# Optimization experiments

Hardware: AMD Instinct MI355X
Metric: run time of the kernel (lower is better)

The kernel has to match this reference:

```python
import jax, jax.numpy as jnp
import numpy as np

B, S, D, H = 2, 2048, 2048, 16
DH = D // H  # 128 head dim
ROPE_THETA = 10000.0
LN_EPS = 1e-5


def setup_inputs() -> dict:
    key = jax.random.key(0)
    k1, k2, k3 = jax.random.split(key, 3)
    positions = jnp.broadcast_to(jnp.arange(S, dtype=jnp.int64), (B, S))
    hidden_states = jax.random.normal(k1, (B, S, D), dtype=jnp.float32)
    w_qkv = jax.random.normal(k2, (D, 3 * D), dtype=jnp.float32) * 0.02
    w_out = jax.random.normal(k3, (D, D), dtype=jnp.float32) * 0.02
    return {"positions": positions, "hidden_states": hidden_states,
            "w_qkv": w_qkv, "w_out": w_out}


def _rope(x, positions):
    # NeoX-style rotary (vLLM get_rope default): rotate split halves.
    # x: [B, S, H, DH], positions: [B, S]
    half = DH // 2
    inv_freq = 1.0 / (ROPE_THETA ** (jnp.arange(0, half, dtype=jnp.float32) / half))
    ang = positions.astype(jnp.float32)[..., None] * inv_freq  # [B, S, half]
    cos = jnp.cos(ang)[:, :, None, :]  # [B, S, 1, half]
    sin = jnp.sin(ang)[:, :, None, :]
    x1, x2 = x[..., :half], x[..., half:]
    return jnp.concatenate([x1 * cos - x2 * sin, x2 * cos + x1 * sin], axis=-1)


def reference(positions, hidden_states, w_qkv, w_out):
    # LayerNorm with no affine params (elementwise_affine=False)
    mu = jnp.mean(hidden_states, axis=-1, keepdims=True)
    var = jnp.mean(jnp.square(hidden_states - mu), axis=-1, keepdims=True)
    x = (hidden_states - mu) * jax.lax.rsqrt(var + LN_EPS)

    qkv = jnp.einsum('bsd,de->bse', x, w_qkv)  # [B, S, 3D]
    q, k, v = jnp.split(qkv, 3, axis=-1)
    q = q.reshape(B, S, H, DH)
    k = k.reshape(B, S, H, DH)
    v = v.reshape(B, S, H, DH)

    q = _rope(q, positions)
    k = _rope(k, positions)

    scale = DH ** -0.5
    scores = jnp.einsum('bqhd,bkhd->bhqk', q, k) * scale  # [B, H, S, S]
    causal = jnp.tril(jnp.ones((S, S), dtype=bool))
    scores = jnp.where(causal, scores, jnp.finfo(scores.dtype).min)
    probs = jax.nn.softmax(scores, axis=-1)
    attn = jnp.einsum('bhqk,bkhd->bqhd', probs, v).reshape(B, S, D)

    return jnp.einsum('bsd,de->bse', attn, w_out)
```

## Files before the change

kernel.cpp:

```cpp
#include <hip/hip_runtime.h>


typedef __bf16 bf16x8 __attribute__((ext_vector_type(8)));
typedef float f32x4 __attribute__((ext_vector_type(4)));

__device__ __forceinline__ unsigned short f2bf(float f) {
  unsigned u = __builtin_bit_cast(unsigned, f);
  u = u + 0x7fffu + ((u >> 16) & 1u);
  return (unsigned short)(u >> 16);
}
__device__ __forceinline__ float bf2f(unsigned short h) {
  unsigned u = ((unsigned)h) << 16;
  return __builtin_bit_cast(float, u);
}

#define GLD_LDS16(gp, lp)                                                      \
  __builtin_amdgcn_global_load_lds((__attribute__((address_space(1))) void*)(gp), \
                                   (__attribute__((address_space(3))) void*)(lp), \
                                   16, 0, 0)

__global__ __launch_bounds__(256) void ln_kernel(const float* __restrict__ hs,
                                                 unsigned short* __restrict__ xb) {
  const int row = blockIdx.x;
  const int tid = threadIdx.x;
  const float* rp = hs + (size_t)row * 2048;
  const float4 v0 = ((const float4*)rp)[tid];
  const float4 v1 = ((const float4*)rp)[tid + 256];
  float s  = v0.x + v0.y + v0.z + v0.w + v1.x + v1.y + v1.z + v1.w;
  float ss = v0.x*v0.x + v0.y*v0.y + v0.z*v0.z + v0.w*v0.w
           + v1.x*v1.x + v1.y*v1.y + v1.z*v1.z + v1.w*v1.w;
#pragma unroll
  for (int m = 1; m < 64; m <<= 1) { s += __shfl_xor(s, m); ss += __shfl_xor(ss, m); }
  __shared__ float rs[4], rss[4];
  if ((tid & 63) == 0) { rs[tid >> 6] = s; rss[tid >> 6] = ss; }
  __syncthreads();
  s  = rs[0] + rs[1] + rs[2] + rs[3];
  ss = rss[0] + rss[1] + rss[2] + rss[3];
  const float mean = s * (1.0f / 2048.0f);
  const float var  = ss * (1.0f / 2048.0f) - mean * mean;
  const float inv  = rsqrtf(var + 1e-5f);
  ushort4 o0, o1;
  o0.x = f2bf((v0.x - mean) * inv); o0.y = f2bf((v0.y - mean) * inv);
  o0.z = f2bf((v0.z - mean) * inv); o0.w = f2bf((v0.w - mean) * inv);
  o1.x = f2bf((v1.x - mean) * inv); o1.y = f2bf((v1.y - mean) * inv);
  o1.z = f2bf((v1.z - mean) * inv); o1.w = f2bf((v1.w - mean) * inv);
  ushort4* op = (ushort4*)(xb + (size_t)row * 2048);
  op[tid] = o0; op[tid + 256] = o1;
}

__global__ __launch_bounds__(256) void cast_transpose(const float* __restrict__ in,
                                                      unsigned short* __restrict__ out,
                                                      int K, int N) {
  __shared__ float t[32][33];
  const int n0 = blockIdx.x * 32, k0 = blockIdx.y * 32;
  const int tx = threadIdx.x, ty = threadIdx.y;
#pragma unroll
  for (int i = 0; i < 4; i++)
    t[ty + i * 8][tx] = in[(size_t)(k0 + ty + i * 8) * N + n0 + tx];
  __syncthreads();
#pragma unroll
  for (int i = 0; i < 4; i++)
    out[(size_t)(n0 + ty + i * 8) * K + k0 + tx] = f2bf(t[tx][ty + i * 8]);
}

template <int OUT_BF16>
__global__ __launch_bounds__(256) void gemm_bt(const unsigned short* __restrict__ A,
                                               const unsigned short* __restrict__ Bt,
                                               void* __restrict__ Cv,
                                               int M, int N, int K) {
  __shared__ alignas(16) unsigned short sA[128 * 32];
  __shared__ alignas(16) unsigned short sB[128 * 32];
  const int tid = threadIdx.x;
  const int lane = tid & 63, wave = tid >> 6;
  const int wm = wave >> 1, wn = wave & 1;
  const int ln15 = lane & 15, quad = lane >> 4;
  const size_t m0 = (size_t)blockIdx.y * 128, n0 = (size_t)blockIdx.x * 128;
  const unsigned short* Ag = A + m0 * (size_t)K;
  const unsigned short* Bg = Bt + n0 * (size_t)K;
  const int c0 = wave * 2, c1 = wave * 2 + 1;
  const int lr = lane >> 2;
  const int scw = ((lane & 3) ^ ((lr >> 1) & 3)) * 8;
  const int rsw = (ln15 >> 1) & 3;

  f32x4 acc[4][4];
#pragma unroll
  for (int mi = 0; mi < 4; mi++)
#pragma unroll
    for (int ni = 0; ni < 4; ni++) acc[mi][ni] = (f32x4){0.f, 0.f, 0.f, 0.f};

  const int iters = K >> 5;
  for (int kt = 0; kt < iters; ++kt) {
    const int kb = kt * 32;
    __syncthreads();
    GLD_LDS16(Ag + (size_t)(c0 * 16 + lr) * K + kb + scw, &sA[c0 * 512]);
    GLD_LDS16(Ag + (size_t)(c1 * 16 + lr) * K + kb + scw, &sA[c1 * 512]);
    GLD_LDS16(Bg + (size_t)(c0 * 16 + lr) * K + kb + scw, &sB[c0 * 512]);
    GLD_LDS16(Bg + (size_t)(c1 * 16 + lr) * K + kb + scw, &sB[c1 * 512]);
    __syncthreads();
    bf16x8 af[4], bf[4];
#pragma unroll
    for (int mi = 0; mi < 4; mi++)
      af[mi] = *(const bf16x8*)&sA[(wm * 64 + mi * 16 + ln15) * 32 + (quad ^ rsw) * 8];
#pragma unroll
    for (int ni = 0; ni < 4; ni++)
      bf[ni] = *(const bf16x8*)&sB[(wn * 64 + ni * 16 + ln15) * 32 + (quad ^ rsw) * 8];
#pragma unroll
    for (int mi = 0; mi < 4; mi++)
#pragma unroll
      for (int ni = 0; ni < 4; ni++)
        acc[mi][ni] = __builtin_amdgcn_mfma_f32_16x16x32_bf16(af[mi], bf[ni], acc[mi][ni], 0, 0, 0);
  }
#pragma unroll
  for (int mi = 0; mi < 4; mi++)
#pragma unroll
    for (int ni = 0; ni < 4; ni++) {
      const size_t col = n0 + wn * 64 + ni * 16 + ln15;
#pragma unroll
      for (int r = 0; r < 4; r++) {
        const size_t row = m0 + wm * 64 + mi * 16 + quad * 4 + r;
        if (OUT_BF16)
          ((unsigned short*)Cv)[row * N + col] = f2bf(acc[mi][ni][r]);
        else
          ((float*)Cv)[row * N + col] = acc[mi][ni][r];
      }
    }
}

__global__ __launch_bounds__(256) void rope_kernel(const unsigned short* __restrict__ qkv,
                                                   unsigned short* __restrict__ Qo,
                                                   unsigned short* __restrict__ Ko) {
  const int t = blockIdx.x * 256 + threadIdx.x;
  const int i = t & 63;
  const int h = (t >> 6) & 15;
  const int row = t >> 10;
  const int s = row & 2047;
  const float freq = exp2f(-(float)i * (13.287712379549449f / 64.0f));
  const float ang = (float)s * freq;
  float rev = ang * 0.15915494309189535f;
  rev -= floorf(rev);
  const float ar = rev * 6.283185307179586f;
  const float sn = __sinf(ar), cs = __cosf(ar);
  const float qscale = 0.08838834764831845f;
  const size_t base = (size_t)row * 6144 + h * 128;
  const float q1 = bf2f(qkv[base + i]);
  const float q2 = bf2f(qkv[base + 64 + i]);
  const float k1 = bf2f(qkv[base + 2048 + i]);
  const float k2 = bf2f(qkv[base + 2048 + 64 + i]);
  const size_t ob = ((size_t)(((row >> 11) << 4) + h) * 2048 + s) * 128;
  Qo[ob + i]      = f2bf((q1 * cs - q2 * sn) * qscale);
  Qo[ob + 64 + i] = f2bf((q2 * cs + q1 * sn) * qscale);
  Ko[ob + i]      = f2bf(k1 * cs - k2 * sn);
  Ko[ob + 64 + i] = f2bf(k2 * cs + k1 * sn);
}

__global__ __launch_bounds__(256) void vtrans_kernel(const unsigned short* __restrict__ qkv,
                                                     unsigned short* __restrict__ VT) {
  __shared__ unsigned short t[32][34];
  const int s0 = blockIdx.x * 32, d0 = blockIdx.y * 32;
  const int bh = blockIdx.z, b = bh >> 4, h = bh & 15;
  const int tx = threadIdx.x, ty = threadIdx.y;
#pragma unroll
  for (int i = 0; i < 4; i++)
    t[ty + i * 8][tx] =
        qkv[(size_t)(b * 2048 + s0 + ty + i * 8) * 6144 + 4096 + h * 128 + d0 + tx];
  __syncthreads();
#pragma unroll
  for (int i = 0; i < 4; i++)
    VT[((size_t)bh * 128 + d0 + ty + i * 8) * 2048 + s0 + tx] = t[tx][ty + i * 8];
}

__global__ __launch_bounds__(256) void flash_kernel(const unsigned short* __restrict__ Q,
                                                    const unsigned short* __restrict__ Kbuf,
                                                    const unsigned short* __restrict__ VT,
                                                    unsigned short* __restrict__ attn) {
  __shared__ alignas(16) unsigned short sK[64 * 128];
  __shared__ alignas(16) unsigned short sVT[128 * 64];
  __shared__ alignas(16) unsigned short sP[64 * 72];

  const int bh = blockIdx.y;
  const int b = bh >> 4, h = bh & 15;
  const int tid = threadIdx.x;
  const int lane = tid & 63, w = tid >> 6;
  const int ln15 = lane & 15, quad = lane >> 4;

  const unsigned short* Qg = Q + (size_t)bh * 2048 * 128;
  const unsigned short* Kg = Kbuf + (size_t)bh * 2048 * 128;
  const unsigned short* Vg = VT + (size_t)bh * 128 * 2048;

  const float L2E = 1.44269504088896f;

#pragma unroll 1
  for (int t = 0; t < 2; t++) {
    const int qt = t ? (31 - (int)blockIdx.x) : (int)blockIdx.x;
    const int q0 = qt * 64;

    bf16x8 qf[4];
#pragma unroll
    for (int ks = 0; ks < 4; ks++)
      qf[ks] = *(const bf16x8*)&Qg[(size_t)(q0 + w * 16 + ln15) * 128 + ks * 32 + quad * 8];

    f32x4 o[8];
#pragma unroll
    for (int nd = 0; nd < 8; nd++) o[nd] = (f32x4){0.f, 0.f, 0.f, 0.f};
    float mrow[4], lrow[4];
#pragma unroll
    for (int r = 0; r < 4; r++) { mrow[r] = -1e30f; lrow[r] = 0.f; }

#pragma unroll 1
    for (int j = 0; j <= qt; j++) {
      const int k0 = j * 64;
      __syncthreads();
#pragma unroll
      for (int i = 0; i < 4; i++) {
        const int c = w * 4 + i;
        const int row = c * 4 + (lane >> 4);
        const int ch = (lane & 15) ^ (row & 15);
        GLD_LDS16(Kg + (size_t)(k0 + row) * 128 + ch * 8, &sK[c * 512]);
      }
#pragma unroll
      for (int i = 0; i < 4; i++) {
        const int c = w * 4 + i;
        const int row = c * 8 + (lane >> 3);
        const int ch = (lane & 7) ^ (row & 7);
        GLD_LDS16(Vg + (size_t)row * 2048 + k0 + ch * 8, &sVT[c * 512]);
      }
      __syncthreads();

      f32x4 sc[4];
#pragma unroll
      for (int ni = 0; ni < 4; ni++) sc[ni] = (f32x4){0.f, 0.f, 0.f, 0.f};
#pragma unroll
      for (int ks = 0; ks < 4; ks++) {
        bf16x8 bk[4];
#pragma unroll
        for (int ni = 0; ni < 4; ni++) {
          const int row = ni * 16 + ln15;
          const int ch = (ks * 4 + quad) ^ (row & 15);
          bk[ni] = *(const bf16x8*)&sK[row * 128 + ch * 8];
        }
#pragma unroll
        for (int ni = 0; ni < 4; ni++)
          sc[ni] = __builtin_amdgcn_mfma_f32_16x16x32_bf16(qf[ks], bk[ni], sc[ni], 0, 0, 0);
      }

      float mt[4] = {-1e30f, -1e30f, -1e30f, -1e30f};
      if (j == qt) {
#pragma unroll
        for (int ni = 0; ni < 4; ni++) {
          const int key = k0 + ni * 16 + ln15;
#pragma unroll
          for (int r = 0; r < 4; r++) {
            const int qrow = q0 + w * 16 + quad * 4 + r;
            float v = sc[ni][r];
            if (key > qrow) v = -1e30f;
            sc[ni][r] = v;
            mt[r] = fmaxf(mt[r], v);
          }
        }
      } else {
#pragma unroll
        for (int ni = 0; ni < 4; ni++)
#pragma unroll
          for (int r = 0; r < 4; r++) mt[r] = fmaxf(mt[r], sc[ni][r]);
      }
#pragma unroll
      for (int r = 0; r < 4; r++) {
        float m = mt[r];
        m = fmaxf(m, __shfl_xor(m, 1));
        m = fmaxf(m, __shfl_xor(m, 2));
        m = fmaxf(m, __shfl_xor(m, 4));
        m = fmaxf(m, __shfl_xor(m, 8));
        const float mnew = fmaxf(mrow[r], m);
        const float alpha = exp2f((mrow[r] - mnew) * L2E);
        mrow[r] = mnew;
        float rs = 0.f;
#pragma unroll
        for (int ni = 0; ni < 4; ni++) {
          const float p = exp2f((sc[ni][r] - mnew) * L2E);
          sc[ni][r] = p;
          rs += p;
        }
        rs += __shfl_xor(rs, 1);
        rs += __shfl_xor(rs, 2);
        rs += __shfl_xor(rs, 4);
        rs += __shfl_xor(rs, 8);
        lrow[r] = lrow[r] * alpha + rs;
#pragma unroll
        for (int nd = 0; nd < 8; nd++) o[nd][r] *= alpha;
      }
#pragma unroll
      for (int ni = 0; ni < 4; ni++)
#pragma unroll
        for (int r = 0; r < 4; r++)
          sP[(w * 16 + quad * 4 + r) * 72 + ni * 16 + ln15] = f2bf(sc[ni][r]);

      bf16x8 pf[2];
#pragma unroll
      for (int kk = 0; kk < 2; kk++)
        pf[kk] = *(const bf16x8*)&sP[(w * 16 + ln15) * 72 + kk * 32 + quad * 8];
#pragma unroll
      for (int kk = 0; kk < 2; kk++)
#pragma unroll
        for (int nd = 0; nd < 8; nd++) {
          const int row = nd * 16 + ln15;
          const int ch = (kk * 4 + quad) ^ (row & 7);
          const bf16x8 bv = *(const bf16x8*)&sVT[row * 64 + ch * 8];
          o[nd] = __builtin_amdgcn_mfma_f32_16x16x32_bf16(pf[kk], bv, o[nd], 0, 0, 0);
        }
    }

#pragma unroll
    for (int r = 0; r < 4; r++) {
      const float inv = 1.0f / lrow[r];
      const int qrow = q0 + w * 16 + quad * 4 + r;
#pragma unroll
      for (int nd = 0; nd < 8; nd++) {
        const int d = nd * 16 + ln15;
        attn[((size_t)(b * 2048 + qrow)) * 2048 + h * 128 + d] = f2bf(o[nd][r] * inv);
      }
    }
  }
}

extern "C" void kernel_launch(void* const* d_in, const int* in_sizes, int n_in,
                              void* d_out, int out_size, void* d_ws, size_t ws_size,
                              hipStream_t stream) {
  const float* hs   = (const float*)d_in[1];
  const float* wqkv = (const float*)d_in[2];
  const float* wout = (const float*)d_in[3];
  float* out = (float*)d_out;
  char* ws = (char*)d_ws;

  unsigned short* x_bf  = (unsigned short*)(ws);
  unsigned short* wqkvT = (unsigned short*)(ws + 16777216);
  unsigned short* woutT = (unsigned short*)(ws + 41943040);
  unsigned short* qkv   = (unsigned short*)(ws + 50331648);
  unsigned short* Qb    = (unsigned short*)(ws + 100663296);
  unsigned short* Kb    = (unsigned short*)(ws + 117440512);
  unsigned short* VT    = wqkvT;
  unsigned short* attn  = x_bf;

  ln_kernel<<<4096, 256, 0, stream>>>(hs, x_bf);
  cast_transpose<<<dim3(192, 64), dim3(32, 8), 0, stream>>>(wqkv, wqkvT, 2048, 6144);
  cast_transpose<<<dim3(64, 64), dim3(32, 8), 0, stream>>>(wout, woutT, 2048, 2048);
  gemm_bt<1><<<dim3(48, 32), 256, 0, stream>>>(x_bf, wqkvT, (void*)qkv, 4096, 6144, 2048);
  rope_kernel<<<16384, 256, 0, stream>>>(qkv, Qb, Kb);
  vtrans_kernel<<<dim3(64, 4, 32), dim3(32, 8), 0, stream>>>(qkv, VT);
  flash_kernel<<<dim3(16, 32), 256, 0, stream>>>(Qb, Kb, VT, attn);
  gemm_bt<0><<<dim3(16, 32), 256, 0, stream>>>(attn, woutT, (void*)out, 4096, 2048, 2048);
}
```

Before: 446.9 us.

## Widen GEMM K-tile, vectorize RoPE, merge weight casts, MFMA row-sum in flash

The GEMM K-tile grows from 32 to 64 with a new XOR swizzle, which halves the barriers and global-load rounds per K step. RoPE now has each thread handle 8 contiguous elements with 16-byte loads and stores, cutting the grid from 16384 to 2048 blocks. The two weight cast-transpose launches become one kernel. In flash attention, the softmax row sum now comes from an extra MFMA against a ones vector instead of shuffle reductions, so it uses bf16-rounded P for the denominator and doubles GEMM LDS use.

Result: faster. 424.7 us (-5.0%).

```diff
diff --git a/kernel.cpp b/kernel.cpp
--- a/kernel.cpp
+++ b/kernel.cpp
@@ -48,11 +48,18 @@
   op[tid] = o0; op[tid + 256] = o1;
 }
 
-__global__ __launch_bounds__(256) void cast_transpose(const float* __restrict__ in,
-                                                      unsigned short* __restrict__ out,
-                                                      int K, int N) {
+__global__ __launch_bounds__(256) void cast_transpose2(const float* __restrict__ wqkv,
+                                                       const float* __restrict__ wout,
+                                                       unsigned short* __restrict__ wqkvT,
+                                                       unsigned short* __restrict__ woutT) {
   __shared__ float t[32][33];
-  const int n0 = blockIdx.x * 32, k0 = blockIdx.y * 32;
+  const int bx = blockIdx.x;
+  const float* in;
+  unsigned short* out;
+  int N, n0;
+  if (bx < 192) { in = wqkv; out = wqkvT; N = 6144; n0 = bx * 32; }
+  else          { in = wout; out = woutT; N = 2048; n0 = (bx - 192) * 32; }
+  const int k0 = blockIdx.y * 32;
   const int tx = threadIdx.x, ty = threadIdx.y;
 #pragma unroll
   for (int i = 0; i < 4; i++)
@@ -60,7 +67,7 @@
   __syncthreads();
 #pragma unroll
   for (int i = 0; i < 4; i++)
-    out[(size_t)(n0 + ty + i * 8) * K + k0 + tx] = f2bf(t[tx][ty + i * 8]);
+    out[(size_t)(n0 + ty + i * 8) * 2048 + k0 + tx] = f2bf(t[tx][ty + i * 8]);
 }
 
 template <int OUT_BF16>
@@ -68,8 +75,8 @@
                                                const unsigned short* __restrict__ Bt,
                                                void* __restrict__ Cv,
                                                int M, int N, int K) {
-  __shared__ alignas(16) unsigned short sA[128 * 32];
-  __shared__ alignas(16) unsigned short sB[128 * 32];
+  __shared__ alignas(16) unsigned short sA[128 * 64];
+  __shared__ alignas(16) unsigned short sB[128 * 64];
   const int tid = threadIdx.x;
   const int lane = tid & 63, wave = tid >> 6;
   const int wm = wave >> 1, wn = wave & 1;
@@ -77,10 +84,9 @@
   const size_t m0 = (size_t)blockIdx.y * 128, n0 = (size_t)blockIdx.x * 128;
   const unsigned short* Ag = A + m0 * (size_t)K;
   const unsigned short* Bg = Bt + n0 * (size_t)K;
-  const int c0 = wave * 2, c1 = wave * 2 + 1;
-  const int lr = lane >> 2;
-  const int scw = ((lane & 3) ^ ((lr >> 1) & 3)) * 8;
-  const int rsw = (ln15 >> 1) & 3;
+  const int lr8 = lane >> 3;
+  const int sc8 = ((lane & 7) ^ (lr8 & 7)) * 8;
+  const int xk = ln15 & 7;
 
   f32x4 acc[4][4];
 #pragma unroll
@@ -88,27 +94,35 @@
 #pragma unroll
     for (int ni = 0; ni < 4; ni++) acc[mi][ni] = (f32x4){0.f, 0.f, 0.f, 0.f};
 
-  const int iters = K >> 5;
+  const int iters = K >> 6;
   for (int kt = 0; kt < iters; ++kt) {
-    const int kb = kt * 32;
+    const int kb = kt * 64;
     __syncthreads();
-    GLD_LDS16(Ag + (size_t)(c0 * 16 + lr) * K + kb + scw, &sA[c0 * 512]);
-    GLD_LDS16(Ag + (size_t)(c1 * 16 + lr) * K + kb + scw, &sA[c1 * 512]);
-    GLD_LDS16(Bg + (size_t)(c0 * 16 + lr) * K + kb + scw, &sB[c0 * 512]);
-    GLD_LDS16(Bg + (size_t)(c1 * 16 + lr) * K + kb + scw, &sB[c1 * 512]);
+#pragma unroll
+    for (int i = 0; i < 4; i++) {
+      const int c = wave * 4 + i;
+      const int row = c * 8 + lr8;
+      GLD_LDS16(Ag + (size_t)row * K + kb + sc8, &sA[c * 512]);
+      GLD_LDS16(Bg + (size_t)row * K + kb + sc8, &sB[c * 512]);
+    }
     __syncthreads();
-    bf16x8 af[4], bf[4];
-#pragma unroll
-    for (int mi = 0; mi < 4; mi++)
-      af[mi] = *(const bf16x8*)&sA[(wm * 64 + mi * 16 + ln15) * 32 + (quad ^ rsw) * 8];
-#pragma unroll
-    for (int ni = 0; ni < 4; ni++)
-      bf[ni] = *(const bf16x8*)&sB[(wn * 64 + ni * 16 + ln15) * 32 + (quad ^ rsw) * 8];
-#pragma unroll
-    for (int mi = 0; mi < 4; mi++)
+#pragma unroll
+    for (int ks = 0; ks < 2; ks++) {
+      bf16x8 af[4], bf[4];
+#pragma unroll
+      for (int mi = 0; mi < 4; mi++)
+        af[mi] = *(const bf16x8*)&sA[(wm * 64 + mi * 16 + ln15) * 64 +
+                                     ((ks * 4 + quad) ^ xk) * 8];
 #pragma unroll
       for (int ni = 0; ni < 4; ni++)
-        acc[mi][ni] = __builtin_amdgcn_mfma_f32_16x16x32_bf16(af[mi], bf[ni], acc[mi][ni], 0, 0, 0);
+        bf[ni] = *(const bf16x8*)&sB[(wn * 64 + ni * 16 + ln15) * 64 +
+                                     ((ks * 4 + quad) ^ xk) * 8];
+#pragma unroll
+      for (int mi = 0; mi < 4; mi++)
+#pragma unroll
+        for (int ni = 0; ni < 4; ni++)
+          acc[mi][ni] = __builtin_amdgcn_mfma_f32_16x16x32_bf16(af[mi], bf[ni], acc[mi][ni], 0, 0, 0);
+    }
   }
 #pragma unroll
   for (int mi = 0; mi < 4; mi++)
@@ -130,27 +144,37 @@
                                                    unsigned short* __restrict__ Qo,
                                                    unsigned short* __restrict__ Ko) {
   const int t = blockIdx.x * 256 + threadIdx.x;
-  const int i = t & 63;
-  const int h = (t >> 6) & 15;
-  const int row = t >> 10;
+  const int g = t & 7;
+  const int h = (t >> 3) & 15;
+  const int row = t >> 7;
   const int s = row & 2047;
-  const float freq = exp2f(-(float)i * (13.287712379549449f / 64.0f));
-  const float ang = (float)s * freq;
-  float rev = ang * 0.15915494309189535f;
-  rev -= floorf(rev);
-  const float ar = rev * 6.283185307179586f;
-  const float sn = __sinf(ar), cs = __cosf(ar);
+  const size_t base = (size_t)row * 6144 + h * 128 + g * 8;
+  const bf16x8 q1 = *(const bf16x8*)&qkv[base];
+  const bf16x8 q2 = *(const bf16x8*)&qkv[base + 64];
+  const bf16x8 k1 = *(const bf16x8*)&qkv[base + 2048];
+  const bf16x8 k2 = *(const bf16x8*)&qkv[base + 2048 + 64];
   const float qscale = 0.08838834764831845f;
-  const size_t base = (size_t)row * 6144 + h * 128;
-  const float q1 = bf2f(qkv[base + i]);
-  const float q2 = bf2f(qkv[base + 64 + i]);
-  const float k1 = bf2f(qkv[base + 2048 + i]);
-  const float k2 = bf2f(qkv[base + 2048 + 64 + i]);
-  const size_t ob = ((size_t)(((row >> 11) << 4) + h) * 2048 + s) * 128;
-  Qo[ob + i]      = f2bf((q1 * cs - q2 * sn) * qscale);
-  Qo[ob + 64 + i] = f2bf((q2 * cs + q1 * sn) * qscale);
-  Ko[ob + i]      = f2bf(k1 * cs - k2 * sn);
-  Ko[ob + 64 + i] = f2bf(k2 * cs + k1 * sn);
+  bf16x8 oq1, oq2, ok1, ok2;
+#pragma unroll
+  for (int j = 0; j < 8; j++) {
+    const int i = g * 8 + j;
+    const float freq = exp2f(-(float)i * (13.287712379549449f / 64.0f));
+    float rev = (float)s * freq * 0.15915494309189535f;
+    rev -= floorf(rev);
+    const float ar = rev * 6.283185307179586f;
+    const float sn = __sinf(ar), cs = __cosf(ar);
+    const float a1 = (float)q1[j], a2 = (float)q2[j];
+    const float b1 = (float)k1[j], b2 = (float)k2[j];
+    oq1[j] = (__bf16)((a1 * cs - a2 * sn) * qscale);
+    oq2[j] = (__bf16)((a2 * cs + a1 * sn) * qscale);
+    ok1[j] = (__bf16)(b1 * cs - b2 * sn);
+    ok2[j] = (__bf16)(b2 * cs + b1 * sn);
+  }
+  const size_t ob = ((size_t)(((row >> 11) << 4) + h) * 2048 + s) * 128 + g * 8;
+  *(bf16x8*)&Qo[ob]      = oq1;
+  *(bf16x8*)&Qo[ob + 64] = oq2;
+  *(bf16x8*)&Ko[ob]      = ok1;
+  *(bf16x8*)&Ko[ob + 64] = ok2;
 }
 
 __global__ __launch_bounds__(256) void vtrans_kernel(const unsigned short* __restrict__ qkv,
@@ -188,6 +212,9 @@
   const unsigned short* Vg = VT + (size_t)bh * 128 * 2048;
 
   const float L2E = 1.44269504088896f;
+  bf16x8 onesf;
+#pragma unroll
+  for (int j = 0; j < 8; j++) onesf[j] = (__bf16)1.0f;
 
 #pragma unroll 1
   for (int t = 0; t < 2; t++) {
@@ -199,12 +226,13 @@
     for (int ks = 0; ks < 4; ks++)
       qf[ks] = *(const bf16x8*)&Qg[(size_t)(q0 + w * 16 + ln15) * 128 + ks * 32 + quad * 8];
 
-    f32x4 o[8];
+    f32x4 o[8], ol;
 #pragma unroll
     for (int nd = 0; nd < 8; nd++) o[nd] = (f32x4){0.f, 0.f, 0.f, 0.f};
-    float mrow[4], lrow[4];
-#pragma unroll
-    for (int r = 0; r < 4; r++) { mrow[r] = -1e30f; lrow[r] = 0.f; }
+    ol = (f32x4){0.f, 0.f, 0.f, 0.f};
+    float mrow[4];
+#pragma unroll
+    for (int r = 0; r < 4; r++) mrow[r] = -1e30f;
 
 #pragma unroll 1
     for (int j = 0; j <= qt; j++) {
@@ -273,18 +301,10 @@
         const float mnew = fmaxf(mrow[r], m);
         const float alpha = exp2f((mrow[r] - mnew) * L2E);
         mrow[r] = mnew;
-        float rs = 0.f;
-#pragma unroll
-        for (int ni = 0; ni < 4; ni++) {
-          const float p = exp2f((sc[ni][r] - mnew) * L2E);
-          sc[ni][r] = p;
-          rs += p;
-        }
-        rs += __shfl_xor(rs, 1);
-        rs += __shfl_xor(rs, 2);
-        rs += __shfl_xor(rs, 4);
-        rs += __shfl_xor(rs, 8);
-        lrow[r] = lrow[r] * alpha + rs;
+#pragma unroll
+        for (int ni = 0; ni < 4; ni++)
+          sc[ni][r] = exp2f((sc[ni][r] - mnew) * L2E);
+        ol[r] *= alpha;
 #pragma unroll
         for (int nd = 0; nd < 8; nd++) o[nd][r] *= alpha;
       }
@@ -299,7 +319,7 @@
       for (int kk = 0; kk < 2; kk++)
         pf[kk] = *(const bf16x8*)&sP[(w * 16 + ln15) * 72 + kk * 32 + quad * 8];
 #pragma unroll
-      for (int kk = 0; kk < 2; kk++)
+      for (int kk = 0; kk < 2; kk++) {
 #pragma unroll
         for (int nd = 0; nd < 8; nd++) {
           const int row = nd * 16 + ln15;
@@ -307,11 +327,13 @@
           const bf16x8 bv = *(const bf16x8*)&sVT[row * 64 + ch * 8];
           o[nd] = __builtin_amdgcn_mfma_f32_16x16x32_bf16(pf[kk], bv, o[nd], 0, 0, 0);
         }
+        ol = __builtin_amdgcn_mfma_f32_16x16x32_bf16(pf[kk], onesf, ol, 0, 0, 0);
+      }
     }
 
 #pragma unroll
     for (int r = 0; r < 4; r++) {
-      const float inv = 1.0f / lrow[r];
+      const float inv = 1.0f / ol[r];
       const int qrow = q0 + w * 16 + quad * 4 + r;
 #pragma unroll
       for (int nd = 0; nd < 8; nd++) {
@@ -341,10 +363,9 @@
   unsigned short* attn  = x_bf;
 
   ln_kernel<<<4096, 256, 0, stream>>>(hs, x_bf);
-  cast_transpose<<<dim3(192, 64), dim3(32, 8), 0, stream>>>(wqkv, wqkvT, 2048, 6144);
-  cast_transpose<<<dim3(64, 64), dim3(32, 8), 0, stream>>>(wout, woutT, 2048, 2048);
+  cast_transpose2<<<dim3(256, 64), dim3(32, 8), 0, stream>>>(wqkv, wout, wqkvT, woutT);
   gemm_bt<1><<<dim3(48, 32), 256, 0, stream>>>(x_bf, wqkvT, (void*)qkv, 4096, 6144, 2048);
-  rope_kernel<<<16384, 256, 0, stream>>>(qkv, Qb, Kb);
+  rope_kernel<<<2048, 256, 0, stream>>>(qkv, Qb, Kb);
   vtrans_kernel<<<dim3(64, 4, 32), dim3(32, 8), 0, stream>>>(qkv, VT);
   flash_kernel<<<dim3(16, 32), 256, 0, stream>>>(Qb, Kb, VT, attn);
   gemm_bt<0><<<dim3(16, 32), 256, 0, stream>>>(attn, woutT, (void*)out, 4096, 2048, 2048);
```
